# Optimization experiments

Hardware: AMD Instinct MI355X
Metric: run time of the kernel (lower is better)

Reference implementation:

```python
import jax, jax.numpy as jnp
import numpy as np


def setup_inputs() -> dict:
    key = jax.random.key(0)
    ingredients = jax.random.normal(key, (16, 1024, 1024), dtype=jnp.float32)
    return {"ingredients": ingredients}


def reference(ingredients) -> jnp.ndarray:
    # ingredients: [B, H, W]
    # Output [B, H, W, 5]: channel 0 = center, 1 = up (j-1), 2 = right (k+1),
    # 3 = down (j+1), 4 = left (k-1). At grid borders the original falls back
    # to the CENTER value (padding = ingredients[i][j][k]), which is exactly
    # edge-replication of the center pixel into the missing neighbor slot.
    x = ingredients
    center = x
    up = jnp.concatenate([x[:, :1, :], x[:, :-1, :]], axis=1)    # row 0 -> its own center
    down = jnp.concatenate([x[:, 1:, :], x[:, -1:, :]], axis=1)  # last row -> its own center
    left = jnp.concatenate([x[:, :, :1], x[:, :, :-1]], axis=2)  # col 0 -> its own center
    right = jnp.concatenate([x[:, :, 1:], x[:, :, -1:]], axis=2) # last col -> its own center
    return jnp.stack([center, up, right, down, left], axis=-1)
```

## Files before the change

### kernel.cpp

```cpp
#include <hip/hip_runtime.h>


__global__ __launch_bounds__(256) void stencil5_kernel(
    const float* __restrict__ in, float* __restrict__ out) {
    constexpr int W = 1024;
    constexpr int H = 1024;

    const int t = blockIdx.x * 256 + threadIdx.x;
    const int row = t >> 8;
    const int k0  = (t & 255) << 2;
    const int j   = row & (H - 1);

    const long base = ((long)row << 10);

    const float* prow = in + base + k0;

    const float4 c = *(const float4*)prow;

    const float* uptr = prow - ((j > 0)     ? W : 0);
    const float* dptr = prow + ((j < H - 1) ? W : 0);
    const float4 u = *(const float4*)uptr;
    const float4 d = *(const float4*)dptr;

    float lx = prow[-(k0 > 0 ? 1 : 0)];
    lx = (k0 > 0) ? lx : c.x;
    float rw = prow[(k0 + 4 < W) ? 4 : 3];
    rw = (k0 + 4 < W) ? rw : c.w;

    float4* o = (float4*)(out + (base + k0) * 5);
    o[0] = make_float4(c.x, u.x, c.y, d.x);
    o[1] = make_float4(lx,  c.y, u.y, c.z);
    o[2] = make_float4(d.y, c.x, c.z, u.z);
    o[3] = make_float4(c.w, d.z, c.y, c.w);
    o[4] = make_float4(u.w, rw,  d.w, c.z);
}

extern "C" void kernel_launch(void* const* d_in, const int* in_sizes, int n_in,
                              void* d_out, int out_size, void* d_ws, size_t ws_size,
                              hipStream_t stream) {
    const float* in = (const float*)d_in[0];
    float* out = (float*)d_out;

    const int n = in_sizes[0];
    const int n_threads = n >> 2;
    const int blocks = n_threads >> 8;

    stencil5_kernel<<<blocks, 256, 0, stream>>>(in, out);
}
```

Measured before the change: 437.7 us.

## March blocks down row strips, staging interleaved output in LDS with nontemporal stores

Each block now handles a 16-row strip of one image. It rotates up/center/down rows in registers, so every input row is loaded once instead of three times. Each wave writes its 5-channel interleaved results to a private LDS slice, then reads them back as fully contiguous float4 lane-strided chunks and emits them with nontemporal stores, aiming for better write coalescing and less cache pollution. The trade-offs are fewer blocks (1024) and a serial per-row loop with only one-row prefetch depth, which could limit memory-level parallelism.

```diff
diff --git a/kernel.cpp b/kernel.cpp
--- a/kernel.cpp
+++ b/kernel.cpp
@@ -1,38 +1,74 @@
 #include <hip/hip_runtime.h>
 
+
+typedef float f4 __attribute__((ext_vector_type(4)));
 
 __global__ __launch_bounds__(256) void stencil5_kernel(
     const float* __restrict__ in, float* __restrict__ out) {
     constexpr int W = 1024;
     constexpr int H = 1024;
+    constexpr int R = 16;
 
-    const int t = blockIdx.x * 256 + threadIdx.x;
-    const int row = t >> 8;
-    const int k0  = (t & 255) << 2;
-    const int j   = row & (H - 1);
+    __shared__ float lds[4 * 1280];
 
-    const long base = ((long)row << 10);
+    const int i  = threadIdx.x;
+    const int wv = i >> 6;
+    const int ln = i & 63;
+    const int k0 = i << 2;
 
-    const float* prow = in + base + k0;
+    const int strip = blockIdx.x;
+    const int img   = strip >> 6;
+    const int j0    = (strip & 63) << 4;
 
-    const float4 c = *(const float4*)prow;
+    const float* pimg = in + ((long)img << 20) + k0;
+    const long   row0 = ((long)img << 10) + j0;
 
-    const float* uptr = prow - ((j > 0)     ? W : 0);
-    const float* dptr = prow + ((j < H - 1) ? W : 0);
-    const float4 u = *(const float4*)uptr;
-    const float4 d = *(const float4*)dptr;
+    const int loff = (k0 > 0)     ? -1 : 0;
+    const int roff = (k0 + 4 < W) ?  4 : 3;
 
-    float lx = prow[-(k0 > 0 ? 1 : 0)];
-    lx = (k0 > 0) ? lx : c.x;
-    float rw = prow[(k0 + 4 < W) ? 4 : 3];
-    rw = (k0 + 4 < W) ? rw : c.w;
+    const float* p0 = pimg + ((long)j0 << 10);
+    float4 c = *(const float4*)p0;
+    float4 u = (j0 > 0) ? *(const float4*)(p0 - W) : c;
+    const float* p1 = p0 + W;
+    float4 d = *(const float4*)p1;
+    float lx  = p0[loff], rw  = p0[roff];
+    float dlx = p1[loff], drw = p1[roff];
 
-    float4* o = (float4*)(out + (base + k0) * 5);
-    o[0] = make_float4(c.x, u.x, c.y, d.x);
-    o[1] = make_float4(lx,  c.y, u.y, c.z);
-    o[2] = make_float4(d.y, c.x, c.z, u.z);
-    o[3] = make_float4(c.w, d.z, c.y, c.w);
-    o[4] = make_float4(u.w, rw,  d.w, c.z);
+    float*    lw = lds + wv * 1280;
+    f4*       l5 = (f4*)(lw + ln * 20);
+    const f4* ls = (const f4*)lw;
+
+    for (int r = 0; r < R; ++r) {
+        const int jr = j0 + r;
+
+        const int jn = jr + 2;
+        const int mf = (jn < H) ? jn : H - 1;
+        const float* pf = pimg + ((long)mf << 10);
+        float4 f  = *(const float4*)pf;
+        float flx = pf[loff], frw = pf[roff];
+
+        const float4 dd  = (jr + 1 < H) ? d : c;
+        const float  lxe = (k0 > 0)     ? lx : c.x;
+        const float  rwe = (k0 + 4 < W) ? rw : c.w;
+
+        l5[0] = f4{c.x,  u.x,  c.y,  dd.x};
+        l5[1] = f4{lxe,  c.y,  u.y,  c.z };
+        l5[2] = f4{dd.y, c.x,  c.z,  u.z };
+        l5[3] = f4{c.w,  dd.z, c.y,  c.w };
+        l5[4] = f4{u.w,  rwe,  dd.w, c.z };
+
+        asm volatile("s_waitcnt lgkmcnt(0)" ::: "memory");
+
+        f4* o4 = (f4*)(out + (row0 + r) * 5120) + wv * 320;
+        #pragma unroll
+        for (int q = 0; q < 5; ++q)
+            __builtin_nontemporal_store(ls[ln + 64 * q], o4 + ln + 64 * q);
+
+        asm volatile("" ::: "memory");
+
+        u = c; c = d; d = f;
+        lx = dlx; rw = drw; dlx = flx; drw = frw;
+    }
 }
 
 extern "C" void kernel_launch(void* const* d_in, const int* in_sizes, int n_in,
@@ -42,8 +78,7 @@
     float* out = (float*)d_out;
 
     const int n = in_sizes[0];
-    const int n_threads = n >> 2;
-    const int blocks = n_threads >> 8;
+    const int blocks = (n >> 10) >> 4;
 
     stencil5_kernel<<<blocks, 256, 0, stream>>>(in, out);
 }
```

Result: faster. 377.2 us (-13.8%).
